# Performance work log

Measured on AMD Instinct MI355X. Metric: run time of the kernel, lower is better.

Reference implementation:

```python
import jax, jax.numpy as jnp
import numpy as np

POINT_SAMPLE_NUM = 4096
CHAMFER_W = 1.0
NORM_W = 0.1
EDGE_W = 0.5
EPS = 1e-12


def _face_geometry(vertices, faces):
    # vertices: [B, V, 3], faces: [F, 3] int -> per-face verts, areas, unit normals
    v0 = vertices[:, faces[:, 0]]  # [B, F, 3]
    v1 = vertices[:, faces[:, 1]]
    v2 = vertices[:, faces[:, 2]]
    cross = jnp.cross(v1 - v0, v2 - v0)            # [B, F, 3]
    area2 = jnp.linalg.norm(cross, axis=-1)        # [B, F] (= 2*area)
    normals = cross / (area2[..., None] + EPS)     # unit face normals
    return v0, v1, v2, 0.5 * area2, normals


def _sample_points(vertices, faces, n_samples, key):
    # area-weighted face sampling + uniform barycentric coords
    B = vertices.shape[0]
    v0, v1, v2, area, normals = _face_geometry(vertices, faces)
    k_face, k_u, k_v = jax.random.split(key, 3)
    logits = jnp.log(area + EPS)                   # [B, F]
    face_idx = jax.random.categorical(k_face, logits[:, None, :], axis=-1,
                                      shape=(B, n_samples))  # [B, N]
    gather = lambda a: jnp.take_along_axis(a, face_idx[..., None], axis=1)
    p0, p1, p2 = gather(v0), gather(v1), gather(v2)           # [B, N, 3]
    u = jax.random.uniform(k_u, (B, n_samples, 1))
    v = jax.random.uniform(k_v, (B, n_samples, 1))
    r1 = jnp.sqrt(u)
    points = (1.0 - r1) * p0 + r1 * (1.0 - v) * p1 + r1 * v * p2  # [B, N, 3]
    point_normals = gather(normals)                                # [B, N, 3]
    return points, point_normals


def _chamfer(x, y):
    # x: [B, N, 3], y: [B, M, 3] -> squared-distance chamfer + nn indices
    x2 = jnp.sum(x * x, axis=-1)                   # [B, N]
    y2 = jnp.sum(y * y, axis=-1)                   # [B, M]
    d2 = x2[:, :, None] + y2[:, None, :] - 2.0 * jnp.einsum('bnd,bmd->bnm', x, y)
    d2 = jnp.maximum(d2, 0.0)
    idx_x2y = jnp.argmin(d2, axis=2)               # [B, N] nearest y for each x
    min_x2y = jnp.min(d2, axis=2)
    min_y2x = jnp.min(d2, axis=1)
    return jnp.mean(min_x2y) + jnp.mean(min_y2x), idx_x2y


def _edge_loss(vertices, faces):
    v0 = vertices[:, faces[:, 0]]
    v1 = vertices[:, faces[:, 1]]
    v2 = vertices[:, faces[:, 2]]
    e = jnp.concatenate([v1 - v0, v2 - v1, v0 - v2], axis=1)  # [B, 3F, 3]
    return jnp.mean(jnp.sum(e * e, axis=-1))


def setup_inputs() -> dict:
    key = jax.random.key(0)
    k1, k2, k3, k4 = jax.random.split(key, 4)
    predicted_vertices = jax.random.normal(k1, (4, 2562, 3), dtype=jnp.float32)
    predicted_faces = jax.random.randint(k2, (5120, 3), 0, 2562, dtype=jnp.int64)
    gt_vertices = jax.random.normal(k3, (4, 6890, 3), dtype=jnp.float32)
    gt_faces = jax.random.randint(k4, (13776, 3), 0, 6890, dtype=jnp.int64)
    return {"predicted_vertices": predicted_vertices,
            "predicted_faces": predicted_faces,
            "gt_vertices": gt_vertices,
            "gt_faces": gt_faces}


def reference(predicted_vertices, predicted_faces, gt_vertices, gt_faces):
    key = jax.random.key(42)
    kp, kg = jax.random.split(key)
    pred_pts, pred_nrm = _sample_points(predicted_vertices, predicted_faces,
                                        POINT_SAMPLE_NUM, kp)
    gt_pts, gt_nrm = _sample_points(gt_vertices, gt_faces, POINT_SAMPLE_NUM, kg)
    chamfer, idx_p2g = _chamfer(pred_pts, gt_pts)
    # normal consistency between each predicted point and its nearest gt point
    matched_gt_nrm = jnp.take_along_axis(gt_nrm, idx_p2g[..., None], axis=1)
    cos = jnp.abs(jnp.sum(pred_nrm * matched_gt_nrm, axis=-1))  # [B, N]
    normal_loss = jnp.mean(1.0 - cos)
    edge_loss = _edge_loss(predicted_vertices, predicted_faces)
    return CHAMFER_W * chamfer + NORM_W * normal_loss + EDGE_W * edge_loss
```

## Files before the change

### kernel.cpp

```cpp
#include <hip/hip_runtime.h>
#include <stdint.h>

constexpr int   kB  = 4;
constexpr int   kNS = 4096;
constexpr int   kVP = 2562;
constexpr int   kFP = 5120;
constexpr int   kVG = 6890;
constexpr int   kFG = 13776;
constexpr float kEPS  = 1e-12f;
constexpr int   kPB  = 256;
constexpr int   kPREP_P = (kB * kFP + 255) / 256;
constexpr int   kPREP_G = (kB * kFG + 255) / 256;

__host__ __device__ inline void tf2x32(uint32_t k0, uint32_t k1,
                                       uint32_t& x0r, uint32_t& x1r) {
  uint32_t ks2 = k0 ^ k1 ^ 0x1BD11BDAu;
  uint32_t x0 = x0r + k0, x1 = x1r + k1;
#define TF_R(r) { x0 += x1; x1 = (x1 << (r)) | (x1 >> (32 - (r))); x1 ^= x0; }
  TF_R(13) TF_R(15) TF_R(26) TF_R(6)
  x0 += k1;  x1 += ks2 + 1u;
  TF_R(17) TF_R(29) TF_R(16) TF_R(24)
  x0 += ks2; x1 += k0 + 2u;
  TF_R(13) TF_R(15) TF_R(26) TF_R(6)
  x0 += k0;  x1 += k1 + 3u;
  TF_R(17) TF_R(29) TF_R(16) TF_R(24)
  x0 += k1;  x1 += ks2 + 4u;
  TF_R(13) TF_R(15) TF_R(26) TF_R(6)
  x0 += ks2; x1 += k0 + 5u;
#undef TF_R
  x0r = x0; x1r = x1;
}

__device__ inline float bits_to_unit(uint32_t b) {
  return __uint_as_float((b >> 9) | 0x3f800000u) - 1.0f;
}

__device__ inline int faces_is64(const int* __restrict__ faces) {
  return (faces[1] == 0 && faces[3] == 0 && faces[5] == 0 && faces[7] == 0) ? 1 : 0;
}
__device__ inline int face_vtx(const int* __restrict__ faces, int f, int c,
                               int is64, int V) {
  int e = f * 3 + c;
  int v = faces[is64 ? (e << 1) : e];
  return v < 0 ? 0 : (v >= V ? V - 1 : v);
}

__global__ void mlk_write_scalar(float* out, float val) {
  if (threadIdx.x == 0 && blockIdx.x == 0) out[0] = val;
}

__global__ __launch_bounds__(256) void mlk_prep_faces2(
    const float* __restrict__ pverts, const int* __restrict__ pfaces,
    const float* __restrict__ gverts, const int* __restrict__ gfaces,
    float* __restrict__ wp, float* __restrict__ np,
    float* __restrict__ wg, float* __restrict__ ng) {
  int which = blockIdx.x >= kPREP_P;
  int blk   = which ? blockIdx.x - kPREP_P : blockIdx.x;
  const float* verts = which ? gverts : pverts;
  const int*   faces = which ? gfaces : pfaces;
  float* warea = which ? wg : wp;
  float* fnrm  = which ? ng : np;
  int V = which ? kVG : kVP;
  int F = which ? kFG : kFP;
  int idx = blk * 256 + threadIdx.x;
  if (idx >= kB * F) return;
  int is64 = faces_is64(faces);
  int b = idx / F, f = idx - b * F;
  int i0 = face_vtx(faces, f, 0, is64, V);
  int i1 = face_vtx(faces, f, 1, is64, V);
  int i2 = face_vtx(faces, f, 2, is64, V);
  const float* vb = verts + (size_t)b * V * 3;
  float ax = vb[i0*3+0], ay = vb[i0*3+1], az = vb[i0*3+2];
  float bx = vb[i1*3+0], by = vb[i1*3+1], bz = vb[i1*3+2];
  float cx = vb[i2*3+0], cy = vb[i2*3+1], cz = vb[i2*3+2];
  float e1x = bx-ax, e1y = by-ay, e1z = bz-az;
  float e2x = cx-ax, e2y = cy-ay, e2z = cz-az;
  float nx = e1y*e2z - e1z*e2y;
  float ny = e1z*e2x - e1x*e2z;
  float nz = e1x*e2y - e1y*e2x;
  float area2 = sqrtf(nx*nx + ny*ny + nz*nz);
  warea[idx] = 0.5f * area2 + kEPS;
  float inv_n = 1.0f / (area2 + kEPS);
  fnrm[3*idx+0] = nx*inv_n;
  fnrm[3*idx+1] = ny*inv_n;
  fnrm[3*idx+2] = nz*inv_n;
}

__global__ __launch_bounds__(256) void mlk_prefix2(
    float* __restrict__ wp, float* __restrict__ wg) {
  int which = blockIdx.x >> 2;
  int b = blockIdx.x & 3, tid = threadIdx.x;
  int F = which ? kFG : kFP;
  float* wb = (which ? wg : wp) + (size_t)b * F;
  int C = (F + 255) / 256;
  int lo = tid * C;
  int hi = lo + C; if (hi > F) hi = F; if (lo > F) lo = F;
  float s = 0.f;
  for (int i = lo; i < hi; ++i) s += wb[i];
  __shared__ float ps[256];
  ps[tid] = s;
  __syncthreads();
  for (int off = 1; off < 256; off <<= 1) {
    float v = (tid >= off) ? ps[tid - off] : 0.f;
    __syncthreads();
    ps[tid] += v;
    __syncthreads();
  }
  float p = ps[tid] - s;
  for (int i = lo; i < hi; ++i) { p += wb[i]; wb[i] = p; }
}

__global__ __launch_bounds__(256) void mlk_sample_gen(
    const float* __restrict__ pverts, const int* __restrict__ pfaces,
    const float* __restrict__ pref_p, const float* __restrict__ fnrm_p,
    float* __restrict__ pred_pts, float* __restrict__ pred_nrm,
    const float* __restrict__ gverts, const int* __restrict__ gfaces,
    const float* __restrict__ pref_g, const float* __restrict__ fnrm_g,
    float* __restrict__ gt_pts, float* __restrict__ gt_nrm,
    uint32_t pf0, uint32_t pf1, uint32_t pu0, uint32_t pu1, uint32_t pv0, uint32_t pv1,
    uint32_t gf0, uint32_t gf1, uint32_t gu0, uint32_t gu1, uint32_t gv0, uint32_t gv1) {
  int which = blockIdx.x >> 5;
  int t = ((blockIdx.x & 31) << 8) + threadIdx.x;
  const float* verts = which ? gverts : pverts;
  const int*   faces = which ? gfaces : pfaces;
  const float* pref  = which ? pref_g : pref_p;
  const float* fnrm  = which ? fnrm_g : fnrm_p;
  float* pts  = which ? gt_pts : pred_pts;
  float* pnrm = which ? gt_nrm : pred_nrm;
  int V = which ? kVG : kVP;
  int F = which ? kFG : kFP;
  uint32_t kf0 = which ? gf0 : pf0, kf1 = which ? gf1 : pf1;
  uint32_t ku0 = which ? gu0 : pu0, ku1 = which ? gu1 : pu1;
  uint32_t kv0 = which ? gv0 : pv0, kv1 = which ? gv1 : pv1;
  int is64 = faces_is64(faces);

  uint32_t fx0 = (uint32_t)t, fx1 = (uint32_t)(t + 8192);
  tf2x32(kf0, kf1, fx0, fx1);
  uint32_t ux0 = (uint32_t)t, ux1 = (uint32_t)(t + 8192);
  tf2x32(ku0, ku1, ux0, ux1);
  uint32_t vx0 = (uint32_t)t, vx1 = (uint32_t)(t + 8192);
  tf2x32(kv0, kv1, vx0, vx1);

#pragma unroll
  for (int half = 0; half < 2; ++half) {
    int i = t + half * 8192;
    int b = i >> 12;
    float uf = bits_to_unit(half ? fx1 : fx0);
    const float* Pb = pref + (size_t)b * F;
    float target = uf * Pb[F - 1];
    int lo = 0, hi = F - 1;
    while (lo < hi) {
      int mid = (lo + hi) >> 1;
      if (Pb[mid] > target) hi = mid; else lo = mid + 1;
    }
    int fid = lo;
    float u = bits_to_unit(half ? ux1 : ux0);
    float v = bits_to_unit(half ? vx1 : vx0);
    const float* vb = verts + (size_t)b * V * 3;
    int i0 = face_vtx(faces, fid, 0, is64, V);
    int i1 = face_vtx(faces, fid, 1, is64, V);
    int i2 = face_vtx(faces, fid, 2, is64, V);
    float r1 = sqrtf(u);
    float w0 = 1.0f - r1, w1 = r1 * (1.0f - v), w2 = r1 * v;
#pragma unroll
    for (int c = 0; c < 3; ++c) {
      pts[i*3+c] = w0 * vb[i0*3+c] + w1 * vb[i1*3+c] + w2 * vb[i2*3+c];
      pnrm[i*3+c] = fnrm[((size_t)b*F + fid)*3 + c];
    }
  }
}

__global__ __launch_bounds__(512) void mlk_chamfer4(
    const float* __restrict__ pred_pts, const float* __restrict__ gt_pts,
    float* __restrict__ min_p2g, float* __restrict__ min_g2p,
    int* __restrict__ idx_p2g) {
  int bid = blockIdx.x;
  int dir = bid >> 8;
  int r   = bid & 255;
  int b   = r >> 6;
  int qc  = r & 63;
  const float* qpts = dir ? gt_pts   : pred_pts;
  const float* rpts = dir ? pred_pts : gt_pts;
  int wave = threadIdx.x >> 6;
  int lane = threadIdx.x & 63;

  __shared__ float4 lpx4[kNS/4], lpy4[kNS/4], lpz4[kNS/4];
  float* lpx = (float*)lpx4; float* lpy = (float*)lpy4; float* lpz = (float*)lpz4;
  const float* rb = rpts + (size_t)b * kNS * 3;
  for (int i = threadIdx.x; i < kNS; i += 512) {
    lpx[i] = rb[3*i+0];
    lpy[i] = rb[3*i+1];
    lpz[i] = rb[3*i+2];
  }
  __syncthreads();

  int q  = qc * 64 + lane;
  int gi = b * kNS + q;
  float px = qpts[gi*3+0], py = qpts[gi*3+1], pz = qpts[gi*3+2];
  int j0 = wave * 128;
  float best; int bidx = 0;

  if (dir == 0) {
    float bA = INFINITY, bB = INFINITY; int iA = 0, iB = 0;
#pragma unroll 2
    for (int j = j0; j < j0 + 128; ++j) {
      float4 X = lpx4[j], Y = lpy4[j], Z = lpz4[j];
      int m = j << 2;
      float dx, dy, dz;
      dx = px-X.x; dy = py-Y.x; dz = pz-Z.x; float d0 = dx*dx+dy*dy+dz*dz;
      dx = px-X.y; dy = py-Y.y; dz = pz-Z.y; float d1 = dx*dx+dy*dy+dz*dz;
      dx = px-X.z; dy = py-Y.z; dz = pz-Z.z; float d2 = dx*dx+dy*dy+dz*dz;
      dx = px-X.w; dy = py-Y.w; dz = pz-Z.w; float d3 = dx*dx+dy*dy+dz*dz;
      if (d0 < bA) { bA = d0; iA = m; }
      if (d1 < bA) { bA = d1; iA = m | 1; }
      if (d2 < bB) { bB = d2; iB = m | 2; }
      if (d3 < bB) { bB = d3; iB = m | 3; }
    }
    if (bB < bA || (bB == bA && iB < iA)) { best = bB; bidx = iB; }
    else                                  { best = bA; bidx = iA; }
  } else {
    float bA = INFINITY, bB = INFINITY;
#pragma unroll 2
    for (int j = j0; j < j0 + 128; ++j) {
      float4 X = lpx4[j], Y = lpy4[j], Z = lpz4[j];
      float dx, dy, dz;
      dx = px-X.x; dy = py-Y.x; dz = pz-Z.x; float d0 = dx*dx+dy*dy+dz*dz;
      dx = px-X.y; dy = py-Y.y; dz = pz-Z.y; float d1 = dx*dx+dy*dy+dz*dz;
      dx = px-X.z; dy = py-Y.z; dz = pz-Z.z; float d2 = dx*dx+dy*dy+dz*dz;
      dx = px-X.w; dy = py-Y.w; dz = pz-Z.w; float d3 = dx*dx+dy*dy+dz*dz;
      bA = fminf(bA, fminf(d0, d1));
      bB = fminf(bB, fminf(d2, d3));
    }
    best = fminf(bA, bB);
  }

  __shared__ float cv[8][64];
  __shared__ int   ci[8][64];
  cv[wave][lane] = best; ci[wave][lane] = bidx;
  __syncthreads();
  if (threadIdx.x < 64) {
    float bv = cv[0][lane]; int bi = ci[0][lane];
#pragma unroll
    for (int wv = 1; wv < 8; ++wv) {
      float v = cv[wv][lane];
      int   i = ci[wv][lane];
      if (v < bv || (v == bv && i < bi)) { bv = v; bi = i; }
    }
    if (dir == 0) { min_p2g[gi] = bv; idx_p2g[gi] = bi; }
    else          { min_g2p[gi] = bv; }
  }
}

__global__ __launch_bounds__(256) void mlk_loss_partial(
    const float* __restrict__ min_p2g, const float* __restrict__ min_g2p,
    const float* __restrict__ pred_nrm, const float* __restrict__ gt_nrm,
    const int* __restrict__ idx_p2g,
    const float* __restrict__ pverts, const int* __restrict__ pfaces,
    float* __restrict__ partial) {
  int tid = threadIdx.x;
  int gidx = blockIdx.x * 256 + tid;
  const int stride = kPB * 256;
  int is64 = faces_is64(pfaces);
  float s1 = 0.f, s2 = 0.f, sc = 0.f, se = 0.f;
  for (int i = gidx; i < kB * kNS; i += stride) {
    s1 += min_p2g[i];
    s2 += min_g2p[i];
    int b = i >> 12;
    int m = idx_p2g[i];
    m = m < 0 ? 0 : (m >= kNS ? kNS - 1 : m);
    const float* pn = pred_nrm + (size_t)i * 3;
    const float* gn = gt_nrm + ((size_t)b * kNS + m) * 3;
    sc += fabsf(pn[0]*gn[0] + pn[1]*gn[1] + pn[2]*gn[2]);
  }
  for (int e = gidx; e < kB * kFP * 3; e += stride) {
    int b = e / (kFP * 3);
    int r = e - b * kFP * 3;
    int f = r / 3, k = r - f * 3;
    int ia, ib;
    if (k == 0)      { ia = face_vtx(pfaces, f, 0, is64, kVP); ib = face_vtx(pfaces, f, 1, is64, kVP); }
    else if (k == 1) { ia = face_vtx(pfaces, f, 1, is64, kVP); ib = face_vtx(pfaces, f, 2, is64, kVP); }
    else             { ia = face_vtx(pfaces, f, 2, is64, kVP); ib = face_vtx(pfaces, f, 0, is64, kVP); }
    const float* vb = pverts + (size_t)b * kVP * 3;
    float dx = vb[ib*3+0] - vb[ia*3+0];
    float dy = vb[ib*3+1] - vb[ia*3+1];
    float dz = vb[ib*3+2] - vb[ia*3+2];
    se += dx*dx + dy*dy + dz*dz;
  }
  __shared__ float r1a[256], r2a[256], r3a[256], r4a[256];
  r1a[tid] = s1; r2a[tid] = s2; r3a[tid] = sc; r4a[tid] = se;
  __syncthreads();
  for (int off = 128; off > 0; off >>= 1) {
    if (tid < off) {
      r1a[tid] += r1a[tid+off];
      r2a[tid] += r2a[tid+off];
      r3a[tid] += r3a[tid+off];
      r4a[tid] += r4a[tid+off];
    }
    __syncthreads();
  }
  if (tid == 0) {
    partial[blockIdx.x*4+0] = r1a[0];
    partial[blockIdx.x*4+1] = r2a[0];
    partial[blockIdx.x*4+2] = r3a[0];
    partial[blockIdx.x*4+3] = r4a[0];
  }
}

__global__ __launch_bounds__(256) void mlk_loss_combine(
    const float* __restrict__ partial, float* __restrict__ out) {
  int tid = threadIdx.x;
  __shared__ float r1a[256], r2a[256], r3a[256], r4a[256];
  r1a[tid] = partial[tid*4+0];
  r2a[tid] = partial[tid*4+1];
  r3a[tid] = partial[tid*4+2];
  r4a[tid] = partial[tid*4+3];
  __syncthreads();
  for (int off = 128; off > 0; off >>= 1) {
    if (tid < off) {
      r1a[tid] += r1a[tid+off];
      r2a[tid] += r2a[tid+off];
      r3a[tid] += r3a[tid+off];
      r4a[tid] += r4a[tid+off];
    }
    __syncthreads();
  }
  if (tid == 0) {
    const float invN = 1.0f / (float)(kB * kNS);
    float chamfer = r1a[0] * invN + r2a[0] * invN;
    float nloss = 1.0f - r3a[0] * invN;
    float eloss = r4a[0] / (float)(kB * kFP * 3);
    out[0] = 1.0f * chamfer + 0.1f * nloss + 0.5f * eloss;
  }
}

extern "C" void kernel_launch(void* const* d_in, const int* in_sizes, int n_in,
                              void* d_out, int out_size, void* d_ws, size_t ws_size,
                              hipStream_t stream) {
  const float* pverts = (const float*)d_in[0];
  const int*   pfaces = (const int*)d_in[1];
  const float* gverts = (const float*)d_in[2];
  const int*   gfaces = (const int*)d_in[3];
  float* out = (float*)d_out;

  const size_t needF =
      (size_t)kB*kFP + (size_t)kB*kFG +
      (size_t)kB*kFP*3 + (size_t)kB*kFG*3 +
      4*(size_t)kB*kNS*3 +
      2*(size_t)kB*kNS +
      (size_t)kPB*4 +
      (size_t)kB*kNS;
  if (ws_size < needF * 4) {
    mlk_write_scalar<<<1, 64, 0, stream>>>(out, -1.0f);
    return;
  }

  uint32_t a0 = 0u, a1 = 2u; tf2x32(0u, 42u, a0, a1);
  uint32_t b0 = 1u, b1 = 3u; tf2x32(0u, 42u, b0, b1);
  uint32_t kp0 = a0, kp1 = b0;
  uint32_t kg0 = a1, kg1 = b1;
  uint32_t kpred[6], kgt[6];
  {
    uint32_t p0 = 0u, p1 = 3u; tf2x32(kp0, kp1, p0, p1);
    uint32_t q0 = 1u, q1 = 4u; tf2x32(kp0, kp1, q0, q1);
    uint32_t r0 = 2u, r1 = 5u; tf2x32(kp0, kp1, r0, r1);
    kpred[0]=p0; kpred[1]=q0; kpred[2]=r0; kpred[3]=p1; kpred[4]=q1; kpred[5]=r1;
  }
  {
    uint32_t p0 = 0u, p1 = 3u; tf2x32(kg0, kg1, p0, p1);
    uint32_t q0 = 1u, q1 = 4u; tf2x32(kg0, kg1, q0, q1);
    uint32_t r0 = 2u, r1 = 5u; tf2x32(kg0, kg1, r0, r1);
    kgt[0]=p0; kgt[1]=q0; kgt[2]=r0; kgt[3]=p1; kgt[4]=q1; kgt[5]=r1;
  }

  float* ws = (float*)d_ws;
  float* pref_p   = ws; ws += kB * kFP;
  float* pref_g   = ws; ws += kB * kFG;
  float* fnrm_p   = ws; ws += kB * kFP * 3;
  float* fnrm_g   = ws; ws += kB * kFG * 3;
  float* pred_pts = ws; ws += kB * kNS * 3;
  float* gt_pts   = ws; ws += kB * kNS * 3;
  float* pred_nrm = ws; ws += kB * kNS * 3;
  float* gt_nrm   = ws; ws += kB * kNS * 3;
  float* min_p2g  = ws; ws += kB * kNS;
  float* min_g2p  = ws; ws += kB * kNS;
  float* partial  = ws; ws += kPB * 4;
  int* idx_p2g = (int*)ws; ws += kB * kNS;

  mlk_prep_faces2<<<kPREP_P + kPREP_G, 256, 0, stream>>>(
      pverts, pfaces, gverts, gfaces, pref_p, fnrm_p, pref_g, fnrm_g);

  mlk_prefix2<<<8, 256, 0, stream>>>(pref_p, pref_g);

  mlk_sample_gen<<<64, 256, 0, stream>>>(
      pverts, pfaces, pref_p, fnrm_p, pred_pts, pred_nrm,
      gverts, gfaces, pref_g, fnrm_g, gt_pts, gt_nrm,
      kpred[0], kpred[1], kpred[2], kpred[3], kpred[4], kpred[5],
      kgt[0],  kgt[1],  kgt[2],  kgt[3],  kgt[4],  kgt[5]);

  mlk_chamfer4<<<512, 512, 0, stream>>>(pred_pts, gt_pts, min_p2g, min_g2p, idx_p2g);

  mlk_loss_partial<<<kPB, 256, 0, stream>>>(min_p2g, min_g2p, pred_nrm, gt_nrm, idx_p2g,
                                            pverts, pfaces, partial);
  mlk_loss_combine<<<1, 256, 0, stream>>>(partial, out);
}
```

Before: 84.87 us.

## Split chamfer reference set in halves, two queries per thread, widen prefix scan

The chamfer kernel now gives each block half of the reference points and 128 queries, with each thread handling two queries so every LDS float4 read is reused twice. Per-half minima and indices are written to doubled workspace buffers and merged in the loss kernel. The prefix-scan kernel also moves from 256 to 1024 threads to shorten each thread's serial chunk. This trades fewer LDS loads per distance, and smaller shared memory per block, for extra register pressure and an additional merge step.

```diff
diff --git a/kernel.cpp b/kernel.cpp
--- a/kernel.cpp
+++ b/kernel.cpp
@@ -11,6 +11,7 @@
 constexpr int   kPB  = 256;
 constexpr int   kPREP_P = (kB * kFP + 255) / 256;
 constexpr int   kPREP_G = (kB * kFG + 255) / 256;
+constexpr int   kHN = kB * kNS;
 
 __host__ __device__ inline void tf2x32(uint32_t k0, uint32_t k1,
                                        uint32_t& x0r, uint32_t& x1r) {
@@ -86,21 +87,21 @@
   fnrm[3*idx+2] = nz*inv_n;
 }
 
-__global__ __launch_bounds__(256) void mlk_prefix2(
+__global__ __launch_bounds__(1024) void mlk_prefix2(
     float* __restrict__ wp, float* __restrict__ wg) {
   int which = blockIdx.x >> 2;
   int b = blockIdx.x & 3, tid = threadIdx.x;
   int F = which ? kFG : kFP;
   float* wb = (which ? wg : wp) + (size_t)b * F;
-  int C = (F + 255) / 256;
+  int C = (F + 1023) / 1024;
   int lo = tid * C;
   int hi = lo + C; if (hi > F) hi = F; if (lo > F) lo = F;
   float s = 0.f;
   for (int i = lo; i < hi; ++i) s += wb[i];
-  __shared__ float ps[256];
+  __shared__ float ps[1024];
   ps[tid] = s;
   __syncthreads();
-  for (int off = 1; off < 256; off <<= 1) {
+  for (int off = 1; off < 1024; off <<= 1) {
     float v = (tid >= off) ? ps[tid - off] : 0.f;
     __syncthreads();
     ps[tid] += v;
@@ -170,91 +171,107 @@
   }
 }
 
-__global__ __launch_bounds__(512) void mlk_chamfer4(
+__global__ __launch_bounds__(256) void mlk_chamfer5(
     const float* __restrict__ pred_pts, const float* __restrict__ gt_pts,
-    float* __restrict__ min_p2g, float* __restrict__ min_g2p,
-    int* __restrict__ idx_p2g) {
+    float* __restrict__ minh_p2g, float* __restrict__ minh_g2p,
+    int* __restrict__ idxh_p2g) {
   int bid = blockIdx.x;
   int dir = bid >> 8;
   int r   = bid & 255;
   int b   = r >> 6;
-  int qc  = r & 63;
+  int rr  = r & 63;
+  int qc  = rr >> 1;
+  int rh  = rr & 1;
   const float* qpts = dir ? gt_pts   : pred_pts;
   const float* rpts = dir ? pred_pts : gt_pts;
   int wave = threadIdx.x >> 6;
   int lane = threadIdx.x & 63;
 
-  __shared__ float4 lpx4[kNS/4], lpy4[kNS/4], lpz4[kNS/4];
+  constexpr int HR = kNS / 2;
+  __shared__ float4 lpx4[HR/4], lpy4[HR/4], lpz4[HR/4];
   float* lpx = (float*)lpx4; float* lpy = (float*)lpy4; float* lpz = (float*)lpz4;
-  const float* rb = rpts + (size_t)b * kNS * 3;
-  for (int i = threadIdx.x; i < kNS; i += 512) {
+  const float* rb = rpts + (size_t)b * kNS * 3 + (size_t)rh * HR * 3;
+  for (int i = threadIdx.x; i < HR; i += 256) {
     lpx[i] = rb[3*i+0];
     lpy[i] = rb[3*i+1];
     lpz[i] = rb[3*i+2];
   }
   __syncthreads();
 
-  int q  = qc * 64 + lane;
-  int gi = b * kNS + q;
-  float px = qpts[gi*3+0], py = qpts[gi*3+1], pz = qpts[gi*3+2];
+  int q0 = qc * 128 + lane;
+  int gq0 = b * kNS + q0;
+  int gq1 = gq0 + 64;
+  float px0 = qpts[gq0*3+0], py0 = qpts[gq0*3+1], pz0 = qpts[gq0*3+2];
+  float px1 = qpts[gq1*3+0], py1 = qpts[gq1*3+1], pz1 = qpts[gq1*3+2];
   int j0 = wave * 128;
-  float best; int bidx = 0;
+  float best0, best1; int bidx0 = 0, bidx1 = 0;
 
   if (dir == 0) {
-    float bA = INFINITY, bB = INFINITY; int iA = 0, iB = 0;
+    float bA0 = INFINITY, bB0 = INFINITY, bA1 = INFINITY, bB1 = INFINITY;
+    int iA0 = 0, iB0 = 0, iA1 = 0, iB1 = 0;
 #pragma unroll 2
     for (int j = j0; j < j0 + 128; ++j) {
       float4 X = lpx4[j], Y = lpy4[j], Z = lpz4[j];
       int m = j << 2;
-      float dx, dy, dz;
-      dx = px-X.x; dy = py-Y.x; dz = pz-Z.x; float d0 = dx*dx+dy*dy+dz*dz;
-      dx = px-X.y; dy = py-Y.y; dz = pz-Z.y; float d1 = dx*dx+dy*dy+dz*dz;
-      dx = px-X.z; dy = py-Y.z; dz = pz-Z.z; float d2 = dx*dx+dy*dy+dz*dz;
-      dx = px-X.w; dy = py-Y.w; dz = pz-Z.w; float d3 = dx*dx+dy*dy+dz*dz;
-      if (d0 < bA) { bA = d0; iA = m; }
-      if (d1 < bA) { bA = d1; iA = m | 1; }
-      if (d2 < bB) { bB = d2; iB = m | 2; }
-      if (d3 < bB) { bB = d3; iB = m | 3; }
-    }
-    if (bB < bA || (bB == bA && iB < iA)) { best = bB; bidx = iB; }
-    else                                  { best = bA; bidx = iA; }
+      float dx, dy, dz, d;
+      dx = px0-X.x; dy = py0-Y.x; dz = pz0-Z.x; d = dx*dx+dy*dy+dz*dz; if (d < bA0) { bA0 = d; iA0 = m; }
+      dx = px0-X.y; dy = py0-Y.y; dz = pz0-Z.y; d = dx*dx+dy*dy+dz*dz; if (d < bA0) { bA0 = d; iA0 = m|1; }
+      dx = px0-X.z; dy = py0-Y.z; dz = pz0-Z.z; d = dx*dx+dy*dy+dz*dz; if (d < bB0) { bB0 = d; iB0 = m|2; }
+      dx = px0-X.w; dy = py0-Y.w; dz = pz0-Z.w; d = dx*dx+dy*dy+dz*dz; if (d < bB0) { bB0 = d; iB0 = m|3; }
+      dx = px1-X.x; dy = py1-Y.x; dz = pz1-Z.x; d = dx*dx+dy*dy+dz*dz; if (d < bA1) { bA1 = d; iA1 = m; }
+      dx = px1-X.y; dy = py1-Y.y; dz = pz1-Z.y; d = dx*dx+dy*dy+dz*dz; if (d < bA1) { bA1 = d; iA1 = m|1; }
+      dx = px1-X.z; dy = py1-Y.z; dz = pz1-Z.z; d = dx*dx+dy*dy+dz*dz; if (d < bB1) { bB1 = d; iB1 = m|2; }
+      dx = px1-X.w; dy = py1-Y.w; dz = pz1-Z.w; d = dx*dx+dy*dy+dz*dz; if (d < bB1) { bB1 = d; iB1 = m|3; }
+    }
+    if (bB0 < bA0 || (bB0 == bA0 && iB0 < iA0)) { best0 = bB0; bidx0 = iB0; } else { best0 = bA0; bidx0 = iA0; }
+    if (bB1 < bA1 || (bB1 == bA1 && iB1 < iA1)) { best1 = bB1; bidx1 = iB1; } else { best1 = bA1; bidx1 = iA1; }
   } else {
-    float bA = INFINITY, bB = INFINITY;
+    float bA0 = INFINITY, bB0 = INFINITY, bA1 = INFINITY, bB1 = INFINITY;
 #pragma unroll 2
     for (int j = j0; j < j0 + 128; ++j) {
       float4 X = lpx4[j], Y = lpy4[j], Z = lpz4[j];
       float dx, dy, dz;
-      dx = px-X.x; dy = py-Y.x; dz = pz-Z.x; float d0 = dx*dx+dy*dy+dz*dz;
-      dx = px-X.y; dy = py-Y.y; dz = pz-Z.y; float d1 = dx*dx+dy*dy+dz*dz;
-      dx = px-X.z; dy = py-Y.z; dz = pz-Z.z; float d2 = dx*dx+dy*dy+dz*dz;
-      dx = px-X.w; dy = py-Y.w; dz = pz-Z.w; float d3 = dx*dx+dy*dy+dz*dz;
-      bA = fminf(bA, fminf(d0, d1));
-      bB = fminf(bB, fminf(d2, d3));
-    }
-    best = fminf(bA, bB);
-  }
-
-  __shared__ float cv[8][64];
-  __shared__ int   ci[8][64];
-  cv[wave][lane] = best; ci[wave][lane] = bidx;
+      dx = px0-X.x; dy = py0-Y.x; dz = pz0-Z.x; float d0 = dx*dx+dy*dy+dz*dz;
+      dx = px0-X.y; dy = py0-Y.y; dz = pz0-Z.y; float d1 = dx*dx+dy*dy+dz*dz;
+      dx = px0-X.z; dy = py0-Y.z; dz = pz0-Z.z; float d2 = dx*dx+dy*dy+dz*dz;
+      dx = px0-X.w; dy = py0-Y.w; dz = pz0-Z.w; float d3 = dx*dx+dy*dy+dz*dz;
+      bA0 = fminf(bA0, fminf(d0, d1));
+      bB0 = fminf(bB0, fminf(d2, d3));
+      dx = px1-X.x; dy = py1-Y.x; dz = pz1-Z.x; d0 = dx*dx+dy*dy+dz*dz;
+      dx = px1-X.y; dy = py1-Y.y; dz = pz1-Z.y; d1 = dx*dx+dy*dy+dz*dz;
+      dx = px1-X.z; dy = py1-Y.z; dz = pz1-Z.z; d2 = dx*dx+dy*dy+dz*dz;
+      dx = px1-X.w; dy = py1-Y.w; dz = pz1-Z.w; d3 = dx*dx+dy*dy+dz*dz;
+      bA1 = fminf(bA1, fminf(d0, d1));
+      bB1 = fminf(bB1, fminf(d2, d3));
+    }
+    best0 = fminf(bA0, bB0);
+    best1 = fminf(bA1, bB1);
+  }
+
+  __shared__ float cv[4][128];
+  __shared__ int   ci[4][128];
+  cv[wave][lane]      = best0; ci[wave][lane]      = bidx0;
+  cv[wave][lane + 64] = best1; ci[wave][lane + 64] = bidx1;
   __syncthreads();
-  if (threadIdx.x < 64) {
-    float bv = cv[0][lane]; int bi = ci[0][lane];
+  if (threadIdx.x < 128) {
+    int ql = threadIdx.x;
+    float bv = cv[0][ql]; int bi = ci[0][ql];
 #pragma unroll
-    for (int wv = 1; wv < 8; ++wv) {
-      float v = cv[wv][lane];
-      int   i = ci[wv][lane];
+    for (int wv = 1; wv < 4; ++wv) {
+      float v = cv[wv][ql];
+      int   i = ci[wv][ql];
       if (v < bv || (v == bv && i < bi)) { bv = v; bi = i; }
     }
-    if (dir == 0) { min_p2g[gi] = bv; idx_p2g[gi] = bi; }
-    else          { min_g2p[gi] = bv; }
+    int gi = rh * kHN + b * kNS + qc * 128 + ql;
+    if (dir == 0) { minh_p2g[gi] = bv; idxh_p2g[gi] = rh * HR + bi; }
+    else          { minh_g2p[gi] = bv; }
   }
 }
 
 __global__ __launch_bounds__(256) void mlk_loss_partial(
-    const float* __restrict__ min_p2g, const float* __restrict__ min_g2p,
+    const float* __restrict__ minh_p2g, const float* __restrict__ minh_g2p,
     const float* __restrict__ pred_nrm, const float* __restrict__ gt_nrm,
-    const int* __restrict__ idx_p2g,
+    const int* __restrict__ idxh_p2g,
     const float* __restrict__ pverts, const int* __restrict__ pfaces,
     float* __restrict__ partial) {
   int tid = threadIdx.x;
@@ -262,11 +279,14 @@
   const int stride = kPB * 256;
   int is64 = faces_is64(pfaces);
   float s1 = 0.f, s2 = 0.f, sc = 0.f, se = 0.f;
-  for (int i = gidx; i < kB * kNS; i += stride) {
-    s1 += min_p2g[i];
-    s2 += min_g2p[i];
+  for (int i = gidx; i < kHN; i += stride) {
+    float v0 = minh_p2g[i], v1 = minh_p2g[kHN + i];
+    int   j0 = idxh_p2g[i], j1 = idxh_p2g[kHN + i];
+    float mv; int m;
+    if (v1 < v0) { mv = v1; m = j1; } else { mv = v0; m = j0; }
+    s1 += mv;
+    s2 += fminf(minh_g2p[i], minh_g2p[kHN + i]);
     int b = i >> 12;
-    int m = idx_p2g[i];
     m = m < 0 ? 0 : (m >= kNS ? kNS - 1 : m);
     const float* pn = pred_nrm + (size_t)i * 3;
     const float* gn = gt_nrm + ((size_t)b * kNS + m) * 3;
@@ -346,9 +366,9 @@
       (size_t)kB*kFP + (size_t)kB*kFG +
       (size_t)kB*kFP*3 + (size_t)kB*kFG*3 +
       4*(size_t)kB*kNS*3 +
-      2*(size_t)kB*kNS +
+      4*(size_t)kHN +
       (size_t)kPB*4 +
-      (size_t)kB*kNS;
+      2*(size_t)kHN;
   if (ws_size < needF * 4) {
     mlk_write_scalar<<<1, 64, 0, stream>>>(out, -1.0f);
     return;
@@ -381,15 +401,15 @@
   float* gt_pts   = ws; ws += kB * kNS * 3;
   float* pred_nrm = ws; ws += kB * kNS * 3;
   float* gt_nrm   = ws; ws += kB * kNS * 3;
-  float* min_p2g  = ws; ws += kB * kNS;
-  float* min_g2p  = ws; ws += kB * kNS;
+  float* minh_p2g = ws; ws += 2 * kHN;
+  float* minh_g2p = ws; ws += 2 * kHN;
   float* partial  = ws; ws += kPB * 4;
-  int* idx_p2g = (int*)ws; ws += kB * kNS;
+  int* idxh_p2g = (int*)ws; ws += 2 * kHN;
 
   mlk_prep_faces2<<<kPREP_P + kPREP_G, 256, 0, stream>>>(
       pverts, pfaces, gverts, gfaces, pref_p, fnrm_p, pref_g, fnrm_g);
 
-  mlk_prefix2<<<8, 256, 0, stream>>>(pref_p, pref_g);
+  mlk_prefix2<<<8, 1024, 0, stream>>>(pref_p, pref_g);
 
   mlk_sample_gen<<<64, 256, 0, stream>>>(
       pverts, pfaces, pref_p, fnrm_p, pred_pts, pred_nrm,
@@ -397,9 +417,9 @@
       kpred[0], kpred[1], kpred[2], kpred[3], kpred[4], kpred[5],
       kgt[0],  kgt[1],  kgt[2],  kgt[3],  kgt[4],  kgt[5]);
 
-  mlk_chamfer4<<<512, 512, 0, stream>>>(pred_pts, gt_pts, min_p2g, min_g2p, idx_p2g);
-
-  mlk_loss_partial<<<kPB, 256, 0, stream>>>(min_p2g, min_g2p, pred_nrm, gt_nrm, idx_p2g,
-                                            pverts, pfaces, partial);
+  mlk_chamfer5<<<512, 256, 0, stream>>>(pred_pts, gt_pts, minh_p2g, minh_g2p, idxh_p2g);
+
+  mlk_loss_partial<<<kPB, 256, 0, stream>>>(minh_p2g, minh_g2p, pred_nrm, gt_nrm,
+                                            idxh_p2g, pverts, pfaces, partial);
   mlk_loss_combine<<<1, 256, 0, stream>>>(partial, out);
 }
```

Result: faster. 70.39 us (-17.1%).
